# Optimization experiments

Measured on AMD Instinct MI355X. Metric: run time of the kernel, lower is better.

The kernel has to match this reference:

```python
import jax, jax.numpy as jnp
import numpy as np

D_MODEL = 1024
NUM_HEADS = 16
D_K = D_MODEL // NUM_HEADS
B, S = 2, 2048


def setup_inputs() -> dict:
    key = jax.random.key(0)
    ks = jax.random.split(key, 11)
    sc = 1.0 / np.sqrt(D_MODEL)
    return {
        "query": jax.random.normal(ks[0], (B, S, D_MODEL), jnp.float32),
        "key": jax.random.normal(ks[1], (B, S, D_MODEL), jnp.float32),
        "value": jax.random.normal(ks[2], (B, S, D_MODEL), jnp.float32),
        "Wq": jax.random.normal(ks[3], (D_MODEL, D_MODEL), jnp.float32) * sc,
        "bq": jnp.zeros((D_MODEL,), jnp.float32),
        "Wk": jax.random.normal(ks[4], (D_MODEL, D_MODEL), jnp.float32) * sc,
        "bk": jnp.zeros((D_MODEL,), jnp.float32),
        "Wv": jax.random.normal(ks[5], (D_MODEL, D_MODEL), jnp.float32) * sc,
        "bv": jnp.zeros((D_MODEL,), jnp.float32),
        "Wo": jax.random.normal(ks[6], (D_MODEL, D_MODEL), jnp.float32) * sc,
        "bo": jnp.zeros((D_MODEL,), jnp.float32),
    }


def reference(query, key, value, Wq, bq, Wk, bk, Wv, bv, Wo, bo):
    b, sq, _ = query.shape
    # projections -> [B, H, S, d_k]
    def split_heads(x):
        return x.reshape(b, -1, NUM_HEADS, D_K).transpose(0, 2, 1, 3)

    q = split_heads(query @ Wq + bq)
    k = split_heads(key @ Wk + bk)
    v = split_heads(value @ Wv + bv)

    scores = jnp.einsum("bhqd,bhkd->bhqk", q, k) / np.sqrt(D_K).astype(np.float32)
    probs = jax.nn.softmax(scores, axis=-1)  # dropout p=0 (eval) -> identity
    attn = jnp.einsum("bhqk,bhkd->bhqd", probs, v)
    attn = attn.transpose(0, 2, 1, 3).reshape(b, sq, D_MODEL)
    out = attn @ Wo + bo
    return out, probs
```

## Files before the change

### kernel.cpp

```cpp
#include <hip/hip_runtime.h>


typedef __bf16 bf16x8 __attribute__((ext_vector_type(8)));
typedef float f32x4 __attribute__((ext_vector_type(4)));

typedef const unsigned int __attribute__((address_space(1))) as1c_uint;
typedef unsigned int __attribute__((address_space(3))) as3_uint;

#define S_LEN 2048
#define DM 1024
#define NH 16
#define DK 64
#define BATCH 2
#define M_ROWS 4096
#define KE 0.18033688f

__device__ __forceinline__ unsigned short f2bfu(float f) {
  union { __bf16 b; unsigned short u; } cv;
  cv.b = (__bf16)f;
  return cv.u;
}

__device__ __forceinline__ void gload_lds16(const void* g, void* l) {
  __builtin_amdgcn_global_load_lds((as1c_uint*)g, (as3_uint*)l, 16, 0, 0);
}

__global__ __launch_bounds__(256) void cvt3_kernel(
    const float* __restrict__ q, const float* __restrict__ k,
    const float* __restrict__ v, unsigned short* __restrict__ oq,
    unsigned short* __restrict__ ok_, unsigned short* __restrict__ ov) {
  const float* in = blockIdx.z == 0 ? q : (blockIdx.z == 1 ? k : v);
  unsigned short* out = blockIdx.z == 0 ? oq : (blockIdx.z == 1 ? ok_ : ov);
  size_t i = (size_t)blockIdx.x * 256 + threadIdx.x;
  float4 f = ((const float4*)in)[i];
  ushort4 u;
  u.x = f2bfu(f.x); u.y = f2bfu(f.y); u.z = f2bfu(f.z); u.w = f2bfu(f.w);
  ((ushort4*)out)[i] = u;
}

__global__ __launch_bounds__(256) void wtrans_kernel(
    const float* __restrict__ w0, const float* __restrict__ w1,
    const float* __restrict__ w2, const float* __restrict__ w3,
    unsigned short* __restrict__ o0, unsigned short* __restrict__ o1,
    unsigned short* __restrict__ o2, unsigned short* __restrict__ o3) {
  const float* W = blockIdx.z == 0 ? w0 : (blockIdx.z == 1 ? w1 : (blockIdx.z == 2 ? w2 : w3));
  unsigned short* WT = blockIdx.z == 0 ? o0 : (blockIdx.z == 1 ? o1 : (blockIdx.z == 2 ? o2 : o3));
  __shared__ float tile[32][33];
  int tx = threadIdx.x & 31, ty = threadIdx.x >> 5;
  int bx = blockIdx.x * 32, by = blockIdx.y * 32;
#pragma unroll
  for (int i = 0; i < 32; i += 8)
    tile[ty + i][tx] = W[(size_t)(by + ty + i) * DM + bx + tx];
  __syncthreads();
#pragma unroll
  for (int i = 0; i < 32; i += 8)
    WT[(size_t)(bx + ty + i) * DM + by + tx] = f2bfu(tile[tx][ty + i]);
}

template <int EPI>
__device__ __forceinline__ void gemm_core(const unsigned short* __restrict__ A,
                                          const unsigned short* __restrict__ BT,
                                          const float* __restrict__ bias,
                                          void* __restrict__ C) {
  __shared__ __attribute__((aligned(16))) unsigned short As[128 * 32];
  __shared__ __attribute__((aligned(16))) unsigned short Bs[128 * 32];
  const int tid = threadIdx.x;
  const int w = tid >> 6, l = tid & 63;
  const int wr = w >> 1, wc = w & 1;
  const int fr = l & 15, fq = l >> 4;
  const int m0 = blockIdx.y * 128, n0 = blockIdx.x * 128;
  const int srow = l >> 2;
  const int sk8 = (l & 3) * 8;
  f32x4 acc[4][4] = {};

  for (int k0 = 0; k0 < DM; k0 += 32) {
#pragma unroll
    for (int c = 0; c < 2; c++) {
      int r = c * 64 + w * 16;
      gload_lds16(A + (size_t)(m0 + r + srow) * DM + k0 + sk8, As + (size_t)r * 32);
      gload_lds16(BT + (size_t)(n0 + r + srow) * DM + k0 + sk8, Bs + (size_t)r * 32);
    }
    __syncthreads();
    bf16x8 af[4], bfv[4];
#pragma unroll
    for (int m = 0; m < 4; m++)
      af[m] = *(const bf16x8*)(As + (size_t)(wr * 64 + m * 16 + fr) * 32 + fq * 8);
#pragma unroll
    for (int n = 0; n < 4; n++)
      bfv[n] = *(const bf16x8*)(Bs + (size_t)(wc * 64 + n * 16 + fr) * 32 + fq * 8);
#pragma unroll
    for (int m = 0; m < 4; m++)
#pragma unroll
      for (int n = 0; n < 4; n++)
        acc[m][n] = __builtin_amdgcn_mfma_f32_16x16x32_bf16(af[m], bfv[n], acc[m][n], 0, 0, 0);
    __syncthreads();
  }

#pragma unroll
  for (int m = 0; m < 4; m++) {
#pragma unroll
    for (int n = 0; n < 4; n++) {
      const int col = n0 + wc * 64 + n * 16 + fr;
      const float bv = bias[col];
#pragma unroll
      for (int j = 0; j < 4; j++) {
        const int row = m0 + wr * 64 + m * 16 + fq * 4 + j;
        const float v = acc[m][n][j] + bv;
        if (EPI == 0) {
          ((float*)C)[(size_t)row * DM + col] = v;
        } else {
          const int b = row >> 11, s = row & (S_LEN - 1);
          const int h = col >> 6, d = col & (DK - 1);
          ((unsigned short*)C)[(((size_t)b * NH + h) * S_LEN + s) * DK + d] = f2bfu(v);
        }
      }
    }
  }
}

__global__ __launch_bounds__(256) void gemm_qkv_kernel(
    const unsigned short* __restrict__ xq, const unsigned short* __restrict__ xk,
    const unsigned short* __restrict__ xv, const unsigned short* __restrict__ wq,
    const unsigned short* __restrict__ wk, const unsigned short* __restrict__ wv,
    const float* __restrict__ bq, const float* __restrict__ bk,
    const float* __restrict__ bv, unsigned short* __restrict__ oq,
    unsigned short* __restrict__ okk, unsigned short* __restrict__ ov) {
  const int z = blockIdx.z;
  const unsigned short* A = z == 0 ? xq : (z == 1 ? xk : xv);
  const unsigned short* BT = z == 0 ? wq : (z == 1 ? wk : wv);
  const float* bias = z == 0 ? bq : (z == 1 ? bk : bv);
  unsigned short* C = z == 0 ? oq : (z == 1 ? okk : ov);
  gemm_core<1>(A, BT, bias, C);
}

__global__ __launch_bounds__(256) void gemm_out_kernel(
    const unsigned short* __restrict__ A, const unsigned short* __restrict__ BT,
    const float* __restrict__ bias, float* __restrict__ C) {
  gemm_core<0>(A, BT, bias, C);
}

__global__ __launch_bounds__(256) void vtrans_kernel(
    const unsigned short* __restrict__ V, unsigned short* __restrict__ VT) {
  __shared__ __attribute__((aligned(16))) unsigned short t[64][72];
  const int bh = blockIdx.y, s0 = blockIdx.x * 64;
  const unsigned short* v = V + ((size_t)bh * S_LEN + s0) * DK;
  const int tid = threadIdx.x;
#pragma unroll
  for (int i = 0; i < 4; i++) {
    int idx = tid + 256 * i;
    int r = idx >> 4, c4 = (idx & 15) * 4;
    *(ushort4*)&t[r][c4] = *(const ushort4*)(v + (size_t)r * DK + c4);
  }
  __syncthreads();
  unsigned short* o = VT + (size_t)bh * DK * S_LEN + s0;
#pragma unroll
  for (int i = 0; i < 4; i++) {
    int idx = tid + 256 * i;
    int d = idx >> 4, s4 = (idx & 15) * 4;
    ushort4 u;
    u.x = t[s4 + 0][d]; u.y = t[s4 + 1][d];
    u.z = t[s4 + 2][d]; u.w = t[s4 + 3][d];
    *(ushort4*)(o + (size_t)d * S_LEN + s4) = u;
  }
}

__global__ __launch_bounds__(256) void attn_kernel(
    const unsigned short* __restrict__ Qp, const unsigned short* __restrict__ Kp,
    const unsigned short* __restrict__ VT, float* __restrict__ probs,
    unsigned short* __restrict__ attnc) {
  const int flat = blockIdx.y * 32 + blockIdx.x;
  const int xcd = flat & 7, r = flat >> 3;
  const int bh = xcd * 4 + (r >> 5);
  const int tile = r & 31;
  const int w = threadIdx.x >> 6, l = threadIdx.x & 63;
  const int fr = l & 15, fq = l >> 4;
  const int q0 = tile * 64 + w * 16;
  const int qrow = q0 + fr;
  const unsigned short* Qh = Qp + (size_t)bh * S_LEN * DK;
  const unsigned short* Kh = Kp + (size_t)bh * S_LEN * DK;
  const unsigned short* Vh = VT + (size_t)bh * DK * S_LEN;
  float* ph = probs + (size_t)bh * S_LEN * S_LEN;

  __shared__ __attribute__((aligned(16))) unsigned short Sb[4][64 * 64];
  __shared__ __attribute__((aligned(16))) float Pf[4][16][68];

  const int srow8 = l >> 3;
  const int sgran = ((l & 7) ^ (l >> 3)) << 3;
  const int kr7 = fr & 7;

  bf16x8 qf[2];
  qf[0] = *(const bf16x8*)(Qh + (size_t)qrow * DK + fq * 8);
  qf[1] = *(const bf16x8*)(Qh + (size_t)qrow * DK + 32 + fq * 8);

  const int NIT = S_LEN / 64;

#define STAGE_P1(itn, buf)                                                    \
  {                                                                           \
    _Pragma("unroll") for (int i = 0; i < 2; i++)                             \
        gload_lds16(Kh + (size_t)((itn) * 64 + w * 16 + i * 8 + srow8) * DK + \
                        sgran,                                                \
                    &Sb[buf][(w * 16 + i * 8) * 64]);                         \
  }

  float ps4[4] = {0.f, 0.f, 0.f, 0.f};
  STAGE_P1(0, 0);
  STAGE_P1(1, 1);
  asm volatile("s_waitcnt vmcnt(2)" : : : "memory");
  __builtin_amdgcn_s_barrier();
  for (int it = 0; it < NIT; ++it) {
    const unsigned short* kcur = &Sb[it % 3][0];
    if (it + 2 < NIT) STAGE_P1(it + 2, (it + 2) % 3);
#pragma unroll
    for (int t = 0; t < 4; t++) {
      const int rk = t * 16 + fr;
      const bf16x8 a0 = *(const bf16x8*)&kcur[rk * 64 + ((fq ^ kr7) << 3)];
      const bf16x8 a1 = *(const bf16x8*)&kcur[rk * 64 + (((fq + 4) ^ kr7) << 3)];
      f32x4 s4 = {0.f, 0.f, 0.f, 0.f};
      s4 = __builtin_amdgcn_mfma_f32_16x16x32_bf16(a0, qf[0], s4, 0, 0, 0);
      s4 = __builtin_amdgcn_mfma_f32_16x16x32_bf16(a1, qf[1], s4, 0, 0, 0);
#pragma unroll
      for (int j = 0; j < 4; j++) ps4[j] += __builtin_amdgcn_exp2f(s4[j] * KE);
    }
    if (it + 1 < NIT) {
      if (it + 2 < NIT) {
        asm volatile("s_waitcnt vmcnt(2)" : : : "memory");
      } else {
        asm volatile("s_waitcnt vmcnt(0)" : : : "memory");
      }
      __builtin_amdgcn_s_barrier();
    }
  }
#undef STAGE_P1
  float psum = (ps4[0] + ps4[1]) + (ps4[2] + ps4[3]);
  psum += __shfl_xor(psum, 16, 64);
  psum += __shfl_xor(psum, 32, 64);
  const float pinv = 1.f / psum;
  __builtin_amdgcn_s_barrier();

  f32x4 oacc[4] = {};
  const int strow = l >> 4;
  const int stcol = (l & 15) * 4;
#pragma unroll
  for (int i = 0; i < 2; i++) {
    gload_lds16(Kh + (size_t)(w * 16 + i * 8 + srow8) * DK + sgran,
                &Sb[0][(w * 16 + i * 8) * 64]);
    gload_lds16(Vh + (size_t)(w * 16 + i * 8 + srow8) * S_LEN + sgran,
                &Sb[2][(w * 16 + i * 8) * 64]);
  }
  asm volatile("s_waitcnt vmcnt(0)" : : : "memory");
  __builtin_amdgcn_s_barrier();
  for (int it = 0; it < S_LEN / 64; ++it) {
    const int cur = it & 1;
    const int skb = it * 64;
    if (it + 1 < S_LEN / 64) {
#pragma unroll
      for (int i = 0; i < 2; i++) {
        gload_lds16(Kh + (size_t)(skb + 64 + w * 16 + i * 8 + srow8) * DK + sgran,
                    &Sb[cur ^ 1][(w * 16 + i * 8) * 64]);
        gload_lds16(Vh + (size_t)(w * 16 + i * 8 + srow8) * S_LEN + (skb + 64) + sgran,
                    &Sb[2 + (cur ^ 1)][(w * 16 + i * 8) * 64]);
      }
    }
#pragma unroll
    for (int sub = 0; sub < 2; sub++) {
#pragma unroll
      for (int t = 0; t < 2; t++) {
        const int rk = sub * 32 + t * 16 + fr;
        const bf16x8 a0 = *(const bf16x8*)&Sb[cur][rk * 64 + ((fq ^ kr7) << 3)];
        const bf16x8 a1 = *(const bf16x8*)&Sb[cur][rk * 64 + (((fq + 4) ^ kr7) << 3)];
        f32x4 s4 = {0.f, 0.f, 0.f, 0.f};
        s4 = __builtin_amdgcn_mfma_f32_16x16x32_bf16(a0, qf[0], s4, 0, 0, 0);
        s4 = __builtin_amdgcn_mfma_f32_16x16x32_bf16(a1, qf[1], s4, 0, 0, 0);
        f32x4 pv;
#pragma unroll
        for (int j = 0; j < 4; j++)
          pv[j] = __builtin_amdgcn_exp2f(s4[j] * KE) * pinv;
        *(f32x4*)&Pf[w][fr][sub * 32 + t * 16 + fq * 4] = pv;
      }
      const f32x4 plo = *(const f32x4*)&Pf[w][fr][sub * 32 + fq * 8];
      const f32x4 phi = *(const f32x4*)&Pf[w][fr][sub * 32 + fq * 8 + 4];
      bf16x8 pa;
#pragma unroll
      for (int j = 0; j < 4; j++) {
        pa[j] = (__bf16)plo[j];
        pa[j + 4] = (__bf16)phi[j];
      }
      __builtin_amdgcn_s_setprio(1);
#pragma unroll
      for (int n = 0; n < 4; n++) {
        const bf16x8 vf =
            *(const bf16x8*)&Sb[2 + cur][(n * 16 + fr) * 64 + (((sub * 4 + fq) ^ kr7) << 3)];
        oacc[n] = __builtin_amdgcn_mfma_f32_16x16x32_bf16(pa, vf, oacc[n], 0, 0, 0);
      }
      __builtin_amdgcn_s_setprio(0);
    }
#pragma unroll
    for (int i = 0; i < 4; i++) {
      const f32x4 pv4 = *(const f32x4*)&Pf[w][4 * i + strow][stcol];
      __builtin_nontemporal_store(
          pv4, (f32x4*)(ph + (size_t)(q0 + 4 * i + strow) * S_LEN + skb + stcol));
    }
    if (it + 1 < S_LEN / 64) {
      asm volatile("s_waitcnt vmcnt(4)" : : : "memory");
      __builtin_amdgcn_s_barrier();
    }
  }

  const int b = bh >> 4, h = bh & (NH - 1);
#pragma unroll
  for (int n = 0; n < 4; n++) {
#pragma unroll
    for (int j = 0; j < 4; j++) {
      const int row = q0 + fq * 4 + j, col = h * DK + n * 16 + fr;
      attnc[(size_t)((size_t)b * S_LEN + row) * DM + col] = f2bfu(oacc[n][j]);
    }
  }
}

extern "C" void kernel_launch(void* const* d_in, const int* in_sizes, int n_in,
                              void* d_out, int out_size, void* d_ws, size_t ws_size,
                              hipStream_t stream) {
  const float* query = (const float*)d_in[0];
  const float* key   = (const float*)d_in[1];
  const float* value = (const float*)d_in[2];
  const float* Wq = (const float*)d_in[3];
  const float* bq = (const float*)d_in[4];
  const float* Wk = (const float*)d_in[5];
  const float* bk = (const float*)d_in[6];
  const float* Wv = (const float*)d_in[7];
  const float* bv = (const float*)d_in[8];
  const float* Wo = (const float*)d_in[9];
  const float* bo = (const float*)d_in[10];

  char* ws = (char*)d_ws;
  const size_t XSZ = (size_t)M_ROWS * DM * 2;
  const size_t WSZ = (size_t)DM * DM * 2;
  unsigned short* xq  = (unsigned short*)(ws);
  unsigned short* xk  = (unsigned short*)(ws + XSZ);
  unsigned short* xv  = (unsigned short*)(ws + 2 * XSZ);
  unsigned short* wtq = (unsigned short*)(ws + 3 * XSZ);
  unsigned short* wtk = (unsigned short*)(ws + 3 * XSZ + WSZ);
  unsigned short* wtv = (unsigned short*)(ws + 3 * XSZ + 2 * WSZ);
  unsigned short* wto = (unsigned short*)(ws + 3 * XSZ + 3 * WSZ);
  unsigned short* qp  = (unsigned short*)(ws + 3 * XSZ + 4 * WSZ);
  unsigned short* kp  = (unsigned short*)(ws + 4 * XSZ + 4 * WSZ);
  unsigned short* vp  = (unsigned short*)(ws + 5 * XSZ + 4 * WSZ);
  unsigned short* vT    = xk;
  unsigned short* attnc = xq;

  float* out = (float*)d_out;
  float* probs = (float*)d_out + (size_t)BATCH * S_LEN * DM;

  cvt3_kernel<<<dim3(4096, 1, 3), 256, 0, stream>>>(query, key, value, xq, xk, xv);
  wtrans_kernel<<<dim3(32, 32, 4), 256, 0, stream>>>(Wq, Wk, Wv, Wo, wtq, wtk, wtv, wto);
  gemm_qkv_kernel<<<dim3(8, 32, 3), 256, 0, stream>>>(xq, xk, xv, wtq, wtk, wtv,
                                                      bq, bk, bv, qp, kp, vp);
  vtrans_kernel<<<dim3(32, 32), 256, 0, stream>>>(vp, vT);
  attn_kernel<<<dim3(32, 32), 256, 0, stream>>>(qp, kp, vT, probs, attnc);
  gemm_out_kernel<<<dim3(8, 32), 256, 0, stream>>>(attnc, wto, bo, out);
}
```

Before: 257.8 us.

## Load V fragments directly to registers and shrink LDS for higher occupancy

```diff
diff --git a/kernel.cpp b/kernel.cpp
--- a/kernel.cpp
+++ b/kernel.cpp
@@ -164,7 +164,7 @@
   }
 }
 
-__global__ __launch_bounds__(256) void attn_kernel(
+__global__ __launch_bounds__(256, 4) void attn_kernel(
     const unsigned short* __restrict__ Qp, const unsigned short* __restrict__ Kp,
     const unsigned short* __restrict__ VT, float* __restrict__ probs,
     unsigned short* __restrict__ attnc) {
@@ -181,7 +181,7 @@
   const unsigned short* Vh = VT + (size_t)bh * DK * S_LEN;
   float* ph = probs + (size_t)bh * S_LEN * S_LEN;
 
-  __shared__ __attribute__((aligned(16))) unsigned short Sb[4][64 * 64];
+  __shared__ __attribute__((aligned(16))) unsigned short Kb[2][64 * 64];
   __shared__ __attribute__((aligned(16))) float Pf[4][16][68];
 
   const int srow8 = l >> 3;
@@ -194,27 +194,26 @@
 
   const int NIT = S_LEN / 64;
 
-#define STAGE_P1(itn, buf)                                                    \
+#define STAGE_K(itn, buf)                                                     \
   {                                                                           \
     _Pragma("unroll") for (int i = 0; i < 2; i++)                             \
         gload_lds16(Kh + (size_t)((itn) * 64 + w * 16 + i * 8 + srow8) * DK + \
                         sgran,                                                \
-                    &Sb[buf][(w * 16 + i * 8) * 64]);                         \
+                    &Kb[buf][(w * 16 + i * 8) * 64]);                         \
   }
 
   float ps4[4] = {0.f, 0.f, 0.f, 0.f};
-  STAGE_P1(0, 0);
-  STAGE_P1(1, 1);
-  asm volatile("s_waitcnt vmcnt(2)" : : : "memory");
+  STAGE_K(0, 0);
+  asm volatile("s_waitcnt vmcnt(0)" : : : "memory");
   __builtin_amdgcn_s_barrier();
   for (int it = 0; it < NIT; ++it) {
-    const unsigned short* kcur = &Sb[it % 3][0];
-    if (it + 2 < NIT) STAGE_P1(it + 2, (it + 2) % 3);
+    const int cur = it & 1;
+    if (it + 1 < NIT) STAGE_K(it + 1, cur ^ 1);
 #pragma unroll
     for (int t = 0; t < 4; t++) {
       const int rk = t * 16 + fr;
-      const bf16x8 a0 = *(const bf16x8*)&kcur[rk * 64 + ((fq ^ kr7) << 3)];
-      const bf16x8 a1 = *(const bf16x8*)&kcur[rk * 64 + (((fq + 4) ^ kr7) << 3)];
+      const bf16x8 a0 = *(const bf16x8*)&Kb[cur][rk * 64 + ((fq ^ kr7) << 3)];
+      const bf16x8 a1 = *(const bf16x8*)&Kb[cur][rk * 64 + (((fq + 4) ^ kr7) << 3)];
       f32x4 s4 = {0.f, 0.f, 0.f, 0.f};
       s4 = __builtin_amdgcn_mfma_f32_16x16x32_bf16(a0, qf[0], s4, 0, 0, 0);
       s4 = __builtin_amdgcn_mfma_f32_16x16x32_bf16(a1, qf[1], s4, 0, 0, 0);
@@ -222,15 +221,10 @@
       for (int j = 0; j < 4; j++) ps4[j] += __builtin_amdgcn_exp2f(s4[j] * KE);
     }
     if (it + 1 < NIT) {
-      if (it + 2 < NIT) {
-        asm volatile("s_waitcnt vmcnt(2)" : : : "memory");
-      } else {
-        asm volatile("s_waitcnt vmcnt(0)" : : : "memory");
-      }
+      asm volatile("s_waitcnt vmcnt(0)" : : : "memory");
       __builtin_amdgcn_s_barrier();
     }
   }
-#undef STAGE_P1
   float psum = (ps4[0] + ps4[1]) + (ps4[2] + ps4[3]);
   psum += __shfl_xor(psum, 16, 64);
   psum += __shfl_xor(psum, 32, 64);
@@ -240,34 +234,28 @@
   f32x4 oacc[4] = {};
   const int strow = l >> 4;
   const int stcol = (l & 15) * 4;
-#pragma unroll
-  for (int i = 0; i < 2; i++) {
-    gload_lds16(Kh + (size_t)(w * 16 + i * 8 + srow8) * DK + sgran,
-                &Sb[0][(w * 16 + i * 8) * 64]);
-    gload_lds16(Vh + (size_t)(w * 16 + i * 8 + srow8) * S_LEN + sgran,
-                &Sb[2][(w * 16 + i * 8) * 64]);
-  }
+  const unsigned short* vbase = Vh + (size_t)fr * S_LEN + fq * 8;
+  STAGE_K(0, 0);
   asm volatile("s_waitcnt vmcnt(0)" : : : "memory");
   __builtin_amdgcn_s_barrier();
-  for (int it = 0; it < S_LEN / 64; ++it) {
+  for (int it = 0; it < NIT; ++it) {
     const int cur = it & 1;
     const int skb = it * 64;
-    if (it + 1 < S_LEN / 64) {
-#pragma unroll
-      for (int i = 0; i < 2; i++) {
-        gload_lds16(Kh + (size_t)(skb + 64 + w * 16 + i * 8 + srow8) * DK + sgran,
-                    &Sb[cur ^ 1][(w * 16 + i * 8) * 64]);
-        gload_lds16(Vh + (size_t)(w * 16 + i * 8 + srow8) * S_LEN + (skb + 64) + sgran,
-                    &Sb[2 + (cur ^ 1)][(w * 16 + i * 8) * 64]);
-      }
-    }
+    bf16x8 vv[2][4];
+#pragma unroll
+    for (int sub = 0; sub < 2; sub++)
+#pragma unroll
+      for (int n = 0; n < 4; n++)
+        vv[sub][n] =
+            *(const bf16x8*)(vbase + (size_t)(n * 16) * S_LEN + skb + sub * 32);
+    if (it + 1 < NIT) STAGE_K(it + 1, cur ^ 1);
 #pragma unroll
     for (int sub = 0; sub < 2; sub++) {
 #pragma unroll
       for (int t = 0; t < 2; t++) {
         const int rk = sub * 32 + t * 16 + fr;
-        const bf16x8 a0 = *(const bf16x8*)&Sb[cur][rk * 64 + ((fq ^ kr7) << 3)];
-        const bf16x8 a1 = *(const bf16x8*)&Sb[cur][rk * 64 + (((fq + 4) ^ kr7) << 3)];
+        const bf16x8 a0 = *(const bf16x8*)&Kb[cur][rk * 64 + ((fq ^ kr7) << 3)];
+        const bf16x8 a1 = *(const bf16x8*)&Kb[cur][rk * 64 + (((fq + 4) ^ kr7) << 3)];
         f32x4 s4 = {0.f, 0.f, 0.f, 0.f};
         s4 = __builtin_amdgcn_mfma_f32_16x16x32_bf16(a0, qf[0], s4, 0, 0, 0);
         s4 = __builtin_amdgcn_mfma_f32_16x16x32_bf16(a1, qf[1], s4, 0, 0, 0);
@@ -287,11 +275,8 @@
       }
       __builtin_amdgcn_s_setprio(1);
 #pragma unroll
-      for (int n = 0; n < 4; n++) {
-        const bf16x8 vf =
-            *(const bf16x8*)&Sb[2 + cur][(n * 16 + fr) * 64 + (((sub * 4 + fq) ^ kr7) << 3)];
-        oacc[n] = __builtin_amdgcn_mfma_f32_16x16x32_bf16(pa, vf, oacc[n], 0, 0, 0);
-      }
+      for (int n = 0; n < 4; n++)
+        oacc[n] = __builtin_amdgcn_mfma_f32_16x16x32_bf16(pa, vv[sub][n], oacc[n], 0, 0, 0);
       __builtin_amdgcn_s_setprio(0);
     }
 #pragma unroll
@@ -300,7 +285,7 @@
       __builtin_nontemporal_store(
           pv4, (f32x4*)(ph + (size_t)(q0 + 4 * i + strow) * S_LEN + skb + stcol));
     }
-    if (it + 1 < S_LEN / 64) {
+    if (it + 1 < NIT) {
       asm volatile("s_waitcnt vmcnt(4)" : : : "memory");
       __builtin_amdgcn_s_barrier();
     }
@@ -315,6 +300,7 @@
       attnc[(size_t)((size_t)b * S_LEN + row) * DM + col] = f2bfu(oacc[n][j]);
     }
   }
+#undef STAGE_K
 }
 
 extern "C" void kernel_launch(void* const* d_in, const int* in_sizes, int n_in,
```

After: 263.1 us. 1.02x slower.
